# Performance work log

Hardware: AMD Instinct MI355X
Metric: run time of the kernel (lower is better)

Reference implementation:

```python
import jax, jax.numpy as jnp
import numpy as np

ATOM_DIM = 34
GAT_DIM = 128
HID_DIM = 256
G_LAYERS = 3
ALPHA = 0.2
NEG_INF = -9e15  # matches torch zero_vec constant


def setup_inputs() -> dict:
    key = jax.random.key(0)
    ks = jax.random.split(key, 10)
    B, N = 64, 512
    compound = jax.random.normal(ks[0], (B, N, ATOM_DIM), dtype=jnp.float32)
    adj = jax.random.randint(ks[1], (B, N, N), 0, 2, dtype=jnp.int32)
    # xavier_uniform gain=1.414 approx: bound = gain*sqrt(6/(fan_in+fan_out))
    def xavier(k, shape, gain=1.414):
        bound = gain * np.sqrt(6.0 / (shape[-2] + shape[-1]))
        return jax.random.uniform(k, shape, jnp.float32, -bound, bound)
    W_stack = xavier(ks[2], (G_LAYERS, ATOM_DIM, GAT_DIM))        # per-layer W
    a_stack = xavier(ks[3], (G_LAYERS, 2 * GAT_DIM, 1))            # per-layer a
    W_out = xavier(ks[4], (G_LAYERS * GAT_DIM, GAT_DIM))           # gat_out.W
    a_out = xavier(ks[5], (2 * GAT_DIM, 1))                        # gat_out.a
    lim = 1.0 / np.sqrt(GAT_DIM)
    Wc = jax.random.uniform(ks[6], (GAT_DIM, HID_DIM), jnp.float32, -lim, lim)  # W_comp weight (in,out)
    bc = jax.random.uniform(ks[7], (HID_DIM,), jnp.float32, -lim, lim)
    return {"compound": compound, "adj": adj, "W_stack": W_stack,
            "a_stack": a_stack, "W_out": W_out, "a_out": a_out,
            "Wc": Wc, "bc": bc}


def _gat_layer(h, adj, W, a, concat):
    # h: [B,N,Fin], adj: [B,N,N], W: [Fin,Fout], a: [2*Fout,1]
    Wh = jnp.einsum('bnf,fg->bng', h, W)                 # [B,N,Fout]
    Fout = W.shape[1]
    # e[b,i,j] = leakyrelu(Wh_i . a1 + Wh_j . a2) == leakyrelu(cat(Wh_i,Wh_j) @ a)
    src = Wh @ a[:Fout, 0]                               # [B,N]
    dst = Wh @ a[Fout:, 0]                               # [B,N]
    e = jax.nn.leaky_relu(src[:, :, None] + dst[:, None, :], ALPHA)  # [B,N,N]
    scores = jnp.where(adj > 0, e, NEG_INF)
    attention = jax.nn.softmax(scores, axis=2)
    h_prime = jnp.einsum('bij,bjf->bif', attention, Wh)  # [B,N,Fout]
    return jax.nn.elu(h_prime) if concat else h_prime


def reference(compound, adj, W_stack, a_stack, W_out, a_out, Wc, bc):
    heads = [_gat_layer(compound, adj, W_stack[l], a_stack[l], concat=True)
             for l in range(G_LAYERS)]
    multi = jnp.concatenate(heads, axis=2)               # [B,N,G_LAYERS*GAT_DIM]
    x = jax.nn.elu(_gat_layer(multi, adj, W_out, a_out, concat=False))
    x = jax.nn.leaky_relu(jnp.einsum('bnf,fh->bnh', x, Wc) + bc, ALPHA)
    return x  # [B,N,HID_DIM]
```

## Files before the change

kernel.cpp:

```cpp
#include <hip/hip_runtime.h>
#include <hip/hip_bf16.h>
#include <math.h>


#define ALPHA 0.2f
#define LOG2E 1.44269504088896f

#if __has_builtin(__builtin_amdgcn_exp2f)
#define EXP2F(x) __builtin_amdgcn_exp2f(x)
#else
extern "C" __device__ float __ocml_exp2_f32(float);
#define EXP2F(x) __ocml_exp2_f32(x)
#endif

typedef __attribute__((ext_vector_type(8))) short s16x8;
typedef __attribute__((ext_vector_type(4))) float f32x4;

__device__ __forceinline__ ushort bf16_rne(float f) {
  union { float f; unsigned u; } v; v.f = f;
  unsigned r = v.u + 0x7FFFu + ((v.u >> 16) & 1u);
  return (ushort)(r >> 16);
}
__device__ __forceinline__ float bf16_tof(ushort h) {
  union { unsigned u; float f; } v; v.u = ((unsigned)h) << 16;
  return v.f;
}
__device__ __forceinline__ void split_store4(
    ushort* __restrict__ ph, ushort* __restrict__ pl,
    float v0, float v1, float v2, float v3) {
  ushort h0 = bf16_rne(v0), h1 = bf16_rne(v1), h2 = bf16_rne(v2), h3 = bf16_rne(v3);
  *(ushort4*)ph = make_ushort4(h0, h1, h2, h3);
  *(ushort4*)pl = make_ushort4(bf16_rne(v0 - bf16_tof(h0)), bf16_rne(v1 - bf16_tof(h1)),
                               bf16_rne(v2 - bf16_tof(h2)), bf16_rne(v3 - bf16_tof(h3)));
}

__device__ __forceinline__ long wht_off(long batch, int c, int j) {
  return batch * 65536 + (long)(c >> 4) * 8192 + (j >> 5) * 512 +
         ((c & 15) << 3) + (((j >> 3) & 3) << 7) + (j & 7);
}

__device__ __forceinline__ long w_frag_off(int c, int j, int Kd) {
  return (long)(c >> 4) * (Kd * 16) + (j >> 5) * 512 +
         ((c & 15) << 3) + (((j >> 3) & 3) << 7) + (j & 7);
}

#define WHT_SLOT 8388608L

__global__ __launch_bounds__(256) void wt_prep(
    const float* __restrict__ W, ushort* __restrict__ TH, ushort* __restrict__ TL,
    const int Kd, const int Nd)
{
  const int idx = blockIdx.x * 256 + threadIdx.x;
  if (idx >= Kd * Nd) return;
  const int k = idx / Nd, n = idx % Nd;
  const float v = W[idx];
  const ushort h = bf16_rne(v);
  const long o = w_frag_off(n, k, Kd);
  TH[o] = h;
  TL[o] = bf16_rne(v - bf16_tof(h));
}

__global__ __launch_bounds__(256) void front_union(
    const float* __restrict__ A, const float* __restrict__ Wst,
    const float* __restrict__ ast,
    ushort* __restrict__ whtBase, float* __restrict__ srcB, float* __restrict__ dstB,
    const int* __restrict__ adj, unsigned* __restrict__ mask,
    const float* __restrict__ W_out, ushort* __restrict__ WoT_H, ushort* __restrict__ WoT_L)
{
  __shared__ float AsT[34][36];
  __shared__ float Ws[34][128];
  const int bid = blockIdx.x;
  const int t = threadIdx.x;

  if (bid >= 3072) {
    if (bid < 5120) {
      const int gid = (bid - 3072) * 256 + t;
      const int4* __restrict__ p = (const int4*)(adj + (long)gid * 32);
      unsigned m = 0;
#pragma unroll
      for (int k = 0; k < 8; k++) {
        const int4 v = p[k];
        m |= (v.x > 0 ? 1u : 0u) << (4 * k);
        m |= (v.y > 0 ? 1u : 0u) << (4 * k + 1);
        m |= (v.z > 0 ? 1u : 0u) << (4 * k + 2);
        m |= (v.w > 0 ? 1u : 0u) << (4 * k + 3);
      }
      mask[gid] = m;
    } else {
      const int idx = (bid - 5120) * 256 + t;
      const int k = idx / 128, n = idx % 128;
      const float v = W_out[idx];
      const ushort h = bf16_rne(v);
      const long o = w_frag_off(n, k, 384);
      WoT_H[o] = h;
      WoT_L[o] = bf16_rne(v - bf16_tof(h));
    }
    return;
  }

  const int l = bid >> 10;
  const float* __restrict__ W = Wst + (long)l * 34 * 128;
  const float* __restrict__ avec = ast + (long)l * 256;
  ushort* __restrict__ whtH = whtBase + (long)l * WHT_SLOT;
  ushort* __restrict__ whtL = whtH + 4194304;
  float* __restrict__ src = srcB + (long)l * 32768;
  float* __restrict__ dst = dstB + (long)l * 32768;
  const long row0 = (long)(bid & 1023) * 32;
  const int cg = t & 31, rg = t >> 5;
  {
    const int r = t >> 3, l8 = t & 7;
#pragma unroll
    for (int q = 0; q < 5; q++) {
      int k = l8 + q * 8;
      if (k < 34) AsT[k][r] = A[(row0 + r) * 34 + k];
    }
  }
  {
    int idx = t;
#pragma unroll
    for (int i = 0; i < 17; i++, idx += 256)
      Ws[idx >> 7][idx & 127] = W[idx];
  }
  __syncthreads();

  float acc[4][4];
#pragma unroll
  for (int r = 0; r < 4; r++)
#pragma unroll
    for (int c = 0; c < 4; c++) acc[r][c] = 0.f;
#pragma unroll 2
  for (int k = 0; k < 34; k++) {
    const float4 wv = *(const float4*)&Ws[k][cg * 4];
    const float4 av = *(const float4*)&AsT[k][rg * 4];
#define GFMA(r, a) \
    acc[r][0] += (a) * wv.x; acc[r][1] += (a) * wv.y; \
    acc[r][2] += (a) * wv.z; acc[r][3] += (a) * wv.w;
    GFMA(0, av.x) GFMA(1, av.y) GFMA(2, av.z) GFMA(3, av.w)
#undef GFMA
  }

  {
    const long batch = row0 >> 9;
    const int j = (int)(row0 & 511) + rg * 4;
#pragma unroll
    for (int cc = 0; cc < 4; cc++) {
      const long o = wht_off(batch, cg * 4 + cc, j);
      split_store4(&whtH[o], &whtL[o], acc[0][cc], acc[1][cc], acc[2][cc], acc[3][cc]);
    }
  }

  const float4 a1 = *(const float4*)&avec[cg * 4];
  const float4 a2 = *(const float4*)&avec[128 + cg * 4];
#pragma unroll
  for (int r = 0; r < 4; r++) {
    float s = acc[r][0]*a1.x + acc[r][1]*a1.y + acc[r][2]*a1.z + acc[r][3]*a1.w;
    float d = acc[r][0]*a2.x + acc[r][1]*a2.y + acc[r][2]*a2.z + acc[r][3]*a2.w;
#pragma unroll
    for (int w = 1; w < 32; w <<= 1) {
      s += __shfl_xor(s, w, 64);
      d += __shfl_xor(d, w, 64);
    }
    if (cg == 0) {
      src[row0 + rg * 4 + r] = s * LOG2E;
      dst[row0 + rg * 4 + r] = d * LOG2E;
    }
  }
}

__global__ __launch_bounds__(256, 4) void fused_attn(
    const unsigned* __restrict__ mask,
    const float* __restrict__ srcB, const float* __restrict__ dstB,
    const ushort* __restrict__ whtBase,
    float* __restrict__ out, const int ostride)
{
  __shared__ ushort As[32][520];
  __shared__ float dstS[544];
  __shared__ float invS[32];
  __shared__ float wredM[4];
  const int t = threadIdx.x;
  const int l = blockIdx.z;
  const float* __restrict__ src = srcB + (long)l * 32768;
  const float* __restrict__ dstv = dstB + (long)l * 32768;
  const ushort* __restrict__ whtH = whtBase + (long)l * WHT_SLOT;
  const ushort* __restrict__ whtL = whtH + 4194304;
  const int ocoff = l * 128;
  const int flat = blockIdx.y * 16 + blockIdx.x;
  const int swz = (flat & 7) * 128 + (flat >> 3);
  const long base = (long)(swz >> 4) * 512;
  const int i0 = (swz & 15) * 32;

  const int wv = t >> 6, lane = t & 63;
  const int m16 = lane & 15, q = lane >> 4;
  const int n0 = wv * 32;
  const ushort* __restrict__ bH = whtH + base * 128 + wv * 16384 + lane * 8;
  const ushort* __restrict__ bL = whtL + base * 128 + wv * 16384 + lane * 8;
  s16x8 pa0H = *(const s16x8*)&bH[0];
  s16x8 pa0L = *(const s16x8*)&bL[0];
  s16x8 pa1H = *(const s16x8*)&bH[8192];
  s16x8 pa1L = *(const s16x8*)&bL[8192];
  s16x8 pb0H = *(const s16x8*)&bH[512];
  s16x8 pb0L = *(const s16x8*)&bL[512];
  s16x8 pb1H = *(const s16x8*)&bH[8192 + 512];
  s16x8 pb1L = *(const s16x8*)&bL[8192 + 512];

  {
    const float d0 = dstv[base + t];
    const float d1 = dstv[base + t + 256];
    dstS[t + (t >> 6) * 4] = d0;
    const int t2 = t + 256;
    dstS[t2 + (t2 >> 6) * 4] = d1;
    float mx = fmaxf(d0, d1);
#pragma unroll
    for (int w = 1; w < 64; w <<= 1) mx = fmaxf(mx, __shfl_xor(mx, w, 64));
    if ((t & 63) == 0) wredM[t >> 6] = mx;
  }
  __syncthreads();
  const float md = fmaxf(fmaxf(wredM[0], wredM[1]), fmaxf(wredM[2], wredM[3]));

  {
    const int r = t >> 3, l8 = t & 7;
    const long i = base + i0 + r;
    const float si = src[i];
    const uint2 mw2 = *(const uint2*)(mask + i * 16 + 2 * l8);
    const float em = si + md;
    const float m = fmaxf(em, ALPHA * em);
    const float* __restrict__ dp = &dstS[l8 * 68];
    const int jb = l8 * 64;
    const int xs = l8 << 3;
    float sum = 0.f;
#pragma unroll
    for (int g = 0; g < 16; g++) {
      const float4 dv = *(const float4*)&dp[g * 4];
      const unsigned w = ((g & 8) ? mw2.y : mw2.x) >> ((g & 7) * 4);
      float e0 = si + dv.x, e1 = si + dv.y, e2 = si + dv.z, e3 = si + dv.w;
      e0 = fmaxf(e0, ALPHA * e0) - m; e1 = fmaxf(e1, ALPHA * e1) - m;
      e2 = fmaxf(e2, ALPHA * e2) - m; e3 = fmaxf(e3, ALPHA * e3) - m;
      float p0 = EXP2F(e0), p1 = EXP2F(e1), p2 = EXP2F(e2), p3 = EXP2F(e3);
      p0 = (w & 1u) ? p0 : 0.f;
      p1 = (w & 2u) ? p1 : 0.f;
      p2 = (w & 4u) ? p2 : 0.f;
      p3 = (w & 8u) ? p3 : 0.f;
      sum += (p0 + p1) + (p2 + p3);
      union { __hip_bfloat162 b; unsigned u; } u01, u23;
      u01.b = __float22bfloat162_rn(make_float2(p0, p1));
      u23.b = __float22bfloat162_rn(make_float2(p2, p3));
      *(uint2*)&As[r][(jb + g * 4) ^ xs] = make_uint2(u01.u, u23.u);
    }
#pragma unroll
    for (int w = 1; w < 8; w <<= 1) sum += __shfl_xor(sum, w, 64);
    if (l8 == 0) invS[r] = 1.f / sum;
  }
  __syncthreads();

  f32x4 acc00 = {0.f,0.f,0.f,0.f}, acc01 = {0.f,0.f,0.f,0.f};
  f32x4 acc10 = {0.f,0.f,0.f,0.f}, acc11 = {0.f,0.f,0.f,0.f};
#pragma unroll
  for (int kp = 0; kp < 8; kp++) {
    {
      const int k0 = ((2 * kp) * 32 + q * 8) ^ (kp << 3);
      const s16x8 a0 = *(const s16x8*)&As[m16][k0];
      const s16x8 a1 = *(const s16x8*)&As[16 + m16][k0];
      acc00 = __builtin_amdgcn_mfma_f32_16x16x32_bf16(a0, pa0H, acc00, 0, 0, 0);
      acc01 = __builtin_amdgcn_mfma_f32_16x16x32_bf16(a0, pa1H, acc01, 0, 0, 0);
      acc10 = __builtin_amdgcn_mfma_f32_16x16x32_bf16(a1, pa0H, acc10, 0, 0, 0);
      acc11 = __builtin_amdgcn_mfma_f32_16x16x32_bf16(a1, pa1H, acc11, 0, 0, 0);
      acc00 = __builtin_amdgcn_mfma_f32_16x16x32_bf16(a0, pa0L, acc00, 0, 0, 0);
      acc01 = __builtin_amdgcn_mfma_f32_16x16x32_bf16(a0, pa1L, acc01, 0, 0, 0);
      acc10 = __builtin_amdgcn_mfma_f32_16x16x32_bf16(a1, pa0L, acc10, 0, 0, 0);
      acc11 = __builtin_amdgcn_mfma_f32_16x16x32_bf16(a1, pa1L, acc11, 0, 0, 0);
      if (kp < 7) {
        const int bo = (2 * kp + 2) * 512;
        pa0H = *(const s16x8*)&bH[bo];
        pa0L = *(const s16x8*)&bL[bo];
        pa1H = *(const s16x8*)&bH[8192 + bo];
        pa1L = *(const s16x8*)&bL[8192 + bo];
      }
    }
    {
      const int k0 = ((2 * kp + 1) * 32 + q * 8) ^ (kp << 3);
      const s16x8 a0 = *(const s16x8*)&As[m16][k0];
      const s16x8 a1 = *(const s16x8*)&As[16 + m16][k0];
      acc00 = __builtin_amdgcn_mfma_f32_16x16x32_bf16(a0, pb0H, acc00, 0, 0, 0);
      acc01 = __builtin_amdgcn_mfma_f32_16x16x32_bf16(a0, pb1H, acc01, 0, 0, 0);
      acc10 = __builtin_amdgcn_mfma_f32_16x16x32_bf16(a1, pb0H, acc10, 0, 0, 0);
      acc11 = __builtin_amdgcn_mfma_f32_16x16x32_bf16(a1, pb1H, acc11, 0, 0, 0);
      acc00 = __builtin_amdgcn_mfma_f32_16x16x32_bf16(a0, pb0L, acc00, 0, 0, 0);
      acc01 = __builtin_amdgcn_mfma_f32_16x16x32_bf16(a0, pb1L, acc01, 0, 0, 0);
      acc10 = __builtin_amdgcn_mfma_f32_16x16x32_bf16(a1, pb0L, acc10, 0, 0, 0);
      acc11 = __builtin_amdgcn_mfma_f32_16x16x32_bf16(a1, pb1L, acc11, 0, 0, 0);
      if (kp < 7) {
        const int bo = (2 * kp + 3) * 512;
        pb0H = *(const s16x8*)&bH[bo];
        pb0L = *(const s16x8*)&bL[bo];
        pb1H = *(const s16x8*)&bH[8192 + bo];
        pb1L = *(const s16x8*)&bL[8192 + bo];
      }
    }
  }
#pragma unroll
  for (int reg = 0; reg < 4; reg++) {
    const int row = q * 4 + reg;
    const float li0 = invS[row], li1 = invS[16 + row];
    float v00 = acc00[reg] * li0, v01 = acc01[reg] * li0;
    float v10 = acc10[reg] * li1, v11 = acc11[reg] * li1;
    v00 = v00 > 0.f ? v00 : __expf(v00) - 1.f;
    v01 = v01 > 0.f ? v01 : __expf(v01) - 1.f;
    v10 = v10 > 0.f ? v10 : __expf(v10) - 1.f;
    v11 = v11 > 0.f ? v11 : __expf(v11) - 1.f;
    float* o0 = out + (base + i0 + row) * (long)ostride + ocoff + n0 + m16;
    float* o1 = out + (base + i0 + 16 + row) * (long)ostride + ocoff + n0 + m16;
    o0[0] = v00; o0[16] = v01;
    o1[0] = v10; o1[16] = v11;
  }
}

template<int K, int KC, int MODE>
__global__ __launch_bounds__(256) void mfma_gemm(
    const float* __restrict__ A,
    const ushort* __restrict__ BTH, const ushort* __restrict__ BTL,
    const float* __restrict__ bias, float* __restrict__ outF,
    ushort* __restrict__ whtH, ushort* __restrict__ whtL,
    const float* __restrict__ avec, float* __restrict__ src, float* __restrict__ dst,
    const int ostride)
{
  constexpr int KP = KC + 8;
  __shared__ ushort AsH[32][KP];
  __shared__ ushort AsL[32][KP];
  __shared__ float sredS[4][32], sredD[4][32];
  const int t = threadIdx.x;
  const long row0 = (long)blockIdx.x * 32;
  const int ncoff = (MODE == 1) ? blockIdx.y * 128 : 0;

  const int wv = t >> 6, lane = t & 63;
  const int m16 = lane & 15, q = lane >> 4;
  const int n0 = wv * 32;
  const ushort* __restrict__ bh0 = BTH + (long)((ncoff + n0) >> 4) * (K * 16) + lane * 8;
  const ushort* __restrict__ bl0 = BTL + (long)((ncoff + n0) >> 4) * (K * 16) + lane * 8;

  f32x4 acc[2][2];
#pragma unroll
  for (int m = 0; m < 2; m++)
#pragma unroll
    for (int n = 0; n < 2; n++) acc[m][n] = (f32x4){0.f, 0.f, 0.f, 0.f};

  for (int kc = 0; kc < K; kc += KC) {
    constexpr int NIT = (32 * KC / 4) / 256;
#pragma unroll
    for (int it = 0; it < NIT; it++) {
      const int idx = t + it * 256;
      const int r = idx / (KC / 4), k4 = idx % (KC / 4);
      const float4 v = *(const float4*)&A[(row0 + r) * (long)K + kc + k4 * 4];
      split_store4(&AsH[r][k4 * 4], &AsL[r][k4 * 4], v.x, v.y, v.z, v.w);
    }
    __syncthreads();
#pragma unroll
    for (int ks = 0; ks < KC / 32; ks++) {
      const int k0 = ks * 32 + q * 8;
      const s16x8 a0H = *(const s16x8*)&AsH[m16][k0];
      const s16x8 a0L = *(const s16x8*)&AsL[m16][k0];
      const s16x8 a1H = *(const s16x8*)&AsH[16 + m16][k0];
      const s16x8 a1L = *(const s16x8*)&AsL[16 + m16][k0];
      const int bo = ((kc >> 5) + ks) * 512;
      const s16x8 b0H = *(const s16x8*)&bh0[bo];
      const s16x8 b0L = *(const s16x8*)&bl0[bo];
      const s16x8 b1H = *(const s16x8*)&bh0[K * 16 + bo];
      const s16x8 b1L = *(const s16x8*)&bl0[K * 16 + bo];
      acc[0][0] = __builtin_amdgcn_mfma_f32_16x16x32_bf16(a0H, b0H, acc[0][0], 0, 0, 0);
      acc[0][1] = __builtin_amdgcn_mfma_f32_16x16x32_bf16(a0H, b1H, acc[0][1], 0, 0, 0);
      acc[1][0] = __builtin_amdgcn_mfma_f32_16x16x32_bf16(a1H, b0H, acc[1][0], 0, 0, 0);
      acc[1][1] = __builtin_amdgcn_mfma_f32_16x16x32_bf16(a1H, b1H, acc[1][1], 0, 0, 0);
      acc[0][0] = __builtin_amdgcn_mfma_f32_16x16x32_bf16(a0L, b0H, acc[0][0], 0, 0, 0);
      acc[0][1] = __builtin_amdgcn_mfma_f32_16x16x32_bf16(a0L, b1H, acc[0][1], 0, 0, 0);
      acc[1][0] = __builtin_amdgcn_mfma_f32_16x16x32_bf16(a1L, b0H, acc[1][0], 0, 0, 0);
      acc[1][1] = __builtin_amdgcn_mfma_f32_16x16x32_bf16(a1L, b1H, acc[1][1], 0, 0, 0);
      acc[0][0] = __builtin_amdgcn_mfma_f32_16x16x32_bf16(a0H, b0L, acc[0][0], 0, 0, 0);
      acc[0][1] = __builtin_amdgcn_mfma_f32_16x16x32_bf16(a0H, b1L, acc[0][1], 0, 0, 0);
      acc[1][0] = __builtin_amdgcn_mfma_f32_16x16x32_bf16(a1H, b0L, acc[1][0], 0, 0, 0);
      acc[1][1] = __builtin_amdgcn_mfma_f32_16x16x32_bf16(a1H, b1L, acc[1][1], 0, 0, 0);
    }
    __syncthreads();
  }

  if (MODE == 0) {
    const long batch = row0 >> 9;
    const int iloc = (int)(row0 & 511);
#pragma unroll
    for (int m = 0; m < 2; m++)
#pragma unroll
      for (int n = 0; n < 2; n++) {
        const int c = n0 + n * 16 + m16;
        const int j = iloc + m * 16 + q * 4;
        const long o = wht_off(batch, c, j);
        const f32x4 v = acc[m][n];
        split_store4(&whtH[o], &whtL[o], v[0], v[1], v[2], v[3]);
      }
    const float a10 = avec[n0 + m16], a11 = avec[n0 + 16 + m16];
    const float a20 = avec[128 + n0 + m16], a21 = avec[128 + n0 + 16 + m16];
#pragma unroll
    for (int m = 0; m < 2; m++) {
#pragma unroll
      for (int reg = 0; reg < 4; reg++) {
        float s = acc[m][0][reg] * a10 + acc[m][1][reg] * a11;
        float d = acc[m][0][reg] * a20 + acc[m][1][reg] * a21;
#pragma unroll
        for (int w = 1; w < 16; w <<= 1) {
          s += __shfl_xor(s, w, 64);
          d += __shfl_xor(d, w, 64);
        }
        if (m16 == 0) {
          const int row = m * 16 + q * 4 + reg;
          sredS[wv][row] = s;
          sredD[wv][row] = d;
        }
      }
    }
    __syncthreads();
    if (t < 32) {
      const float s = sredS[0][t] + sredS[1][t] + sredS[2][t] + sredS[3][t];
      const float d = sredD[0][t] + sredD[1][t] + sredD[2][t] + sredD[3][t];
      src[row0 + t] = s * LOG2E;
      dst[row0 + t] = d * LOG2E;
    }
  } else {
#pragma unroll
    for (int m = 0; m < 2; m++)
#pragma unroll
      for (int n = 0; n < 2; n++) {
        const int c = ncoff + n0 + n * 16 + m16;
        const float bv = bias[c];
#pragma unroll
        for (int reg = 0; reg < 4; reg++) {
          float v = acc[m][n][reg] + bv;
          v = fmaxf(v, ALPHA * v);
          outF[(row0 + m * 16 + q * 4 + reg) * (long)ostride + c] = v;
        }
      }
  }
}

extern "C" void kernel_launch(void* const* d_in, const int* in_sizes, int n_in,
                              void* d_out, int out_size, void* d_ws, size_t ws_size,
                              hipStream_t stream) {
  const float* compound = (const float*)d_in[0];
  const int*   adj      = (const int*)d_in[1];
  const float* W_stack  = (const float*)d_in[2];
  const float* a_stack  = (const float*)d_in[3];
  const float* W_out    = (const float*)d_in[4];
  const float* a_out    = (const float*)d_in[5];
  const float* Wc       = (const float*)d_in[6];
  const float* bc       = (const float*)d_in[7];
  float* out = (float*)d_out;

  ushort* wht_all = (ushort*)d_ws;
  float* f     = (float*)d_ws;
  float* multi = f + 12582912;
  float* x     = multi;
  ushort* WcT_H = (ushort*)(multi + 5000000);
  ushort* WcT_L = WcT_H + 32768;

  unsigned* mask = (unsigned*)d_out;
  float* doutF = (float*)d_out;
  float* srcB = doutF + 524288;
  float* dstB = srcB + 4 * 32768;
  ushort* WoT_H = (ushort*)(dstB + 4 * 32768);
  ushort* WoT_L = WoT_H + 98304;
  float* src3 = srcB + 3 * 32768;
  float* dst3 = dstB + 3 * 32768;

  front_union<<<5312, 256, 0, stream>>>(
      compound, W_stack, a_stack, wht_all, srcB, dstB,
      adj, mask, W_out, WoT_H, WoT_L);
  fused_attn<<<dim3(16, 64, 3), 256, 0, stream>>>(
      mask, srcB, dstB, wht_all, multi, 384);
  mfma_gemm<384, 192, 0><<<1024, 256, 0, stream>>>(
      multi, WoT_H, WoT_L, nullptr, nullptr, wht_all, wht_all + 4194304,
      a_out, src3, dst3, 0);
  fused_attn<<<dim3(16, 64, 1), 256, 0, stream>>>(
      mask, src3, dst3, wht_all, x, 128);
  wt_prep<<<128, 256, 0, stream>>>(Wc, WcT_H, WcT_L, 128, 256);
  mfma_gemm<128, 128, 1><<<dim3(1024, 2), 256, 0, stream>>>(
      x, WcT_H, WcT_L, bc, out, nullptr, nullptr, nullptr, nullptr, nullptr, 256);
}
```

Measured before the change: 241.5 us.

## Deepen B-fragment prefetch to four stages and interleave front_union block roles

The attention kernel's register prefetch of the Wh fragments goes from two stages to four, so global loads for k-block KB+4 are issued while block KB's MFMAs run. This hides more load latency but roughly doubles the prefetch register footprint, which under launch_bounds(256,4) may cause spills. Separately, front_union now groups blocks in units of 83 (48 projection, 32 mask-packing, 3 W_out conversion) instead of contiguous ranges. This mixes compute-heavy and bandwidth-heavy blocks across the device at the same time.

```diff
diff --git a/kernel.cpp b/kernel.cpp
--- a/kernel.cpp
+++ b/kernel.cpp
@@ -69,12 +69,13 @@
 {
   __shared__ float AsT[34][36];
   __shared__ float Ws[34][128];
-  const int bid = blockIdx.x;
   const int t = threadIdx.x;
-
-  if (bid >= 3072) {
-    if (bid < 5120) {
-      const int gid = (bid - 3072) * 256 + t;
+  const int g = blockIdx.x / 83, r83 = blockIdx.x - g * 83;
+
+  if (r83 >= 48) {
+    if (r83 < 80) {
+      const int mb = g * 32 + (r83 - 48);
+      const int gid = mb * 256 + t;
       const int4* __restrict__ p = (const int4*)(adj + (long)gid * 32);
       unsigned m = 0;
 #pragma unroll
@@ -87,7 +88,8 @@
       }
       mask[gid] = m;
     } else {
-      const int idx = (bid - 5120) * 256 + t;
+      const int wb = g * 3 + (r83 - 80);
+      const int idx = wb * 256 + t;
       const int k = idx / 128, n = idx % 128;
       const float v = W_out[idx];
       const ushort h = bf16_rne(v);
@@ -98,6 +100,7 @@
     return;
   }
 
+  const int bid = g * 48 + r83;
   const int l = bid >> 10;
   const float* __restrict__ W = Wst + (long)l * 34 * 128;
   const float* __restrict__ avec = ast + (long)l * 256;
@@ -166,6 +169,25 @@
     }
   }
 }
+
+
+#define LD_SET(S, KB) \
+  S##0H = *(const s16x8*)&bH[(KB) * 512]; \
+  S##0L = *(const s16x8*)&bL[(KB) * 512]; \
+  S##1H = *(const s16x8*)&bH[8192 + (KB) * 512]; \
+  S##1L = *(const s16x8*)&bL[8192 + (KB) * 512];
+
+#define MF(a, b, c) c = __builtin_amdgcn_mfma_f32_16x16x32_bf16(a, b, c, 0, 0, 0)
+
+#define STEP(S, KB) { \
+  const int k0_ = ((KB) * 32 + q * 8) ^ ((((KB) >> 1) & 7) << 3); \
+  const s16x8 a0_ = *(const s16x8*)&As[m16][k0_]; \
+  const s16x8 a1_ = *(const s16x8*)&As[16 + m16][k0_]; \
+  MF(a0_, S##0H, acc00); MF(a0_, S##1H, acc01); \
+  MF(a1_, S##0H, acc10); MF(a1_, S##1H, acc11); \
+  MF(a0_, S##0L, acc00); MF(a0_, S##1L, acc01); \
+  MF(a1_, S##0L, acc10); MF(a1_, S##1L, acc11); \
+  if ((KB) + 4 < 16) { LD_SET(S, (KB) + 4) } }
 
 __global__ __launch_bounds__(256, 4) void fused_attn(
     const unsigned* __restrict__ mask,
@@ -194,14 +216,12 @@
   const int n0 = wv * 32;
   const ushort* __restrict__ bH = whtH + base * 128 + wv * 16384 + lane * 8;
   const ushort* __restrict__ bL = whtL + base * 128 + wv * 16384 + lane * 8;
-  s16x8 pa0H = *(const s16x8*)&bH[0];
-  s16x8 pa0L = *(const s16x8*)&bL[0];
-  s16x8 pa1H = *(const s16x8*)&bH[8192];
-  s16x8 pa1L = *(const s16x8*)&bL[8192];
-  s16x8 pb0H = *(const s16x8*)&bH[512];
-  s16x8 pb0L = *(const s16x8*)&bL[512];
-  s16x8 pb1H = *(const s16x8*)&bH[8192 + 512];
-  s16x8 pb1L = *(const s16x8*)&bL[8192 + 512];
+  s16x8 sA0H, sA0L, sA1H, sA1L, sB0H, sB0L, sB1H, sB1L;
+  s16x8 sC0H, sC0L, sC1H, sC1L, sD0H, sD0L, sD1H, sD1L;
+  LD_SET(sA, 0)
+  LD_SET(sB, 1)
+  LD_SET(sC, 2)
+  LD_SET(sD, 3)
 
   {
     const float d0 = dstv[base + t];
@@ -255,47 +275,11 @@
   f32x4 acc00 = {0.f,0.f,0.f,0.f}, acc01 = {0.f,0.f,0.f,0.f};
   f32x4 acc10 = {0.f,0.f,0.f,0.f}, acc11 = {0.f,0.f,0.f,0.f};
 #pragma unroll
-  for (int kp = 0; kp < 8; kp++) {
-    {
-      const int k0 = ((2 * kp) * 32 + q * 8) ^ (kp << 3);
-      const s16x8 a0 = *(const s16x8*)&As[m16][k0];
-      const s16x8 a1 = *(const s16x8*)&As[16 + m16][k0];
-      acc00 = __builtin_amdgcn_mfma_f32_16x16x32_bf16(a0, pa0H, acc00, 0, 0, 0);
-      acc01 = __builtin_amdgcn_mfma_f32_16x16x32_bf16(a0, pa1H, acc01, 0, 0, 0);
-      acc10 = __builtin_amdgcn_mfma_f32_16x16x32_bf16(a1, pa0H, acc10, 0, 0, 0);
-      acc11 = __builtin_amdgcn_mfma_f32_16x16x32_bf16(a1, pa1H, acc11, 0, 0, 0);
-      acc00 = __builtin_amdgcn_mfma_f32_16x16x32_bf16(a0, pa0L, acc00, 0, 0, 0);
-      acc01 = __builtin_amdgcn_mfma_f32_16x16x32_bf16(a0, pa1L, acc01, 0, 0, 0);
-      acc10 = __builtin_amdgcn_mfma_f32_16x16x32_bf16(a1, pa0L, acc10, 0, 0, 0);
-      acc11 = __builtin_amdgcn_mfma_f32_16x16x32_bf16(a1, pa1L, acc11, 0, 0, 0);
-      if (kp < 7) {
-        const int bo = (2 * kp + 2) * 512;
-        pa0H = *(const s16x8*)&bH[bo];
-        pa0L = *(const s16x8*)&bL[bo];
-        pa1H = *(const s16x8*)&bH[8192 + bo];
-        pa1L = *(const s16x8*)&bL[8192 + bo];
-      }
-    }
-    {
-      const int k0 = ((2 * kp + 1) * 32 + q * 8) ^ (kp << 3);
-      const s16x8 a0 = *(const s16x8*)&As[m16][k0];
-      const s16x8 a1 = *(const s16x8*)&As[16 + m16][k0];
-      acc00 = __builtin_amdgcn_mfma_f32_16x16x32_bf16(a0, pb0H, acc00, 0, 0, 0);
-      acc01 = __builtin_amdgcn_mfma_f32_16x16x32_bf16(a0, pb1H, acc01, 0, 0, 0);
-      acc10 = __builtin_amdgcn_mfma_f32_16x16x32_bf16(a1, pb0H, acc10, 0, 0, 0);
-      acc11 = __builtin_amdgcn_mfma_f32_16x16x32_bf16(a1, pb1H, acc11, 0, 0, 0);
-      acc00 = __builtin_amdgcn_mfma_f32_16x16x32_bf16(a0, pb0L, acc00, 0, 0, 0);
-      acc01 = __builtin_amdgcn_mfma_f32_16x16x32_bf16(a0, pb1L, acc01, 0, 0, 0);
-      acc10 = __builtin_amdgcn_mfma_f32_16x16x32_bf16(a1, pb0L, acc10, 0, 0, 0);
-      acc11 = __builtin_amdgcn_mfma_f32_16x16x32_bf16(a1, pb1L, acc11, 0, 0, 0);
-      if (kp < 7) {
-        const int bo = (2 * kp + 3) * 512;
-        pb0H = *(const s16x8*)&bH[bo];
-        pb0L = *(const s16x8*)&bL[bo];
-        pb1H = *(const s16x8*)&bH[8192 + bo];
-        pb1L = *(const s16x8*)&bL[8192 + bo];
-      }
-    }
+  for (int kp = 0; kp < 4; kp++) {
+    STEP(sA, 4 * kp)
+    STEP(sB, 4 * kp + 1)
+    STEP(sC, 4 * kp + 2)
+    STEP(sD, 4 * kp + 3)
   }
 #pragma unroll
   for (int reg = 0; reg < 4; reg++) {
```

Result: faster. 230.9 us (-4.4%).
